# Performance work log

Measured on AMD Instinct MI355X. Metric: run time of the kernel, lower is better.

The kernel has to match this reference:

```python
import jax, jax.numpy as jnp
import numpy as np

K = 64  # init kwarg k
B, D = 4096, 16384


def setup_inputs() -> dict:
    key = jax.random.key(0)
    x = jax.random.normal(key, (B, D), dtype=jnp.float32)
    return {"x": x}


def reference(x):
    # top-k along last dim, then scatter values into a zero tensor (same as
    # torch.topk + zeros_like + scatter_).
    vals, idx = jax.lax.top_k(x, K)            # [B, K], [B, K]
    rows = jnp.arange(x.shape[0])[:, None]     # [B, 1] broadcast against idx
    return jnp.zeros_like(x).at[rows, idx].set(vals)
```

## Files before the change

kernel.cpp:

```cpp
#include <hip/hip_runtime.h>


#define TK_D      16384
#define TK_K      64
#define TK_BLOCK  512
#define TK_NV     8
#define TK_BINS   2048
#define TK_CAP    1024

__device__ __forceinline__ unsigned ord_map(unsigned b) {
    return b ^ ((unsigned)((int)b >> 31) | 0x80000000u);
}
__device__ __forceinline__ unsigned ord_inv(unsigned u) {
    return u ^ ((unsigned)((int)(~u) >> 31) | 0x80000000u);
}

__launch_bounds__(TK_BLOCK, 4)
__global__ void topk_scatter_kernel(const float* __restrict__ x,
                                    float* __restrict__ out) {
    __shared__ int      sh_hist[TK_BINS];
    __shared__ int      sh_wsum[8];
    __shared__ unsigned sh_cu[TK_CAP];
    __shared__ int      sh_cidx[TK_CAP];
    __shared__ int      sh_bin;
    __shared__ int      sh_rem;
    __shared__ int      sh_cnt;
    __shared__ unsigned sh_T;
    __shared__ int      sh_need;

    const int row  = blockIdx.x;
    const int tid  = threadIdx.x;
    const int lane = tid & 63;
    const int wv   = tid >> 6;

    const uint4* __restrict__ xr = (const uint4*)(x + (size_t)row * TK_D);
    uint4 r[TK_NV];
    #pragma unroll
    for (int i = 0; i < TK_NV; i++) r[i] = xr[tid + i * TK_BLOCK];

    ((int4*)sh_hist)[tid] = int4{0, 0, 0, 0};
    if (tid == 0) sh_cnt = 0;

    #pragma unroll
    for (int i = 0; i < TK_NV; i++) {
        r[i].x = ord_map(r[i].x);
        r[i].y = ord_map(r[i].y);
        r[i].z = ord_map(r[i].z);
        r[i].w = ord_map(r[i].w);
    }
    __syncthreads();

    #pragma unroll
    for (int i = 0; i < TK_NV; i++) {
        #pragma unroll
        for (int c = 0; c < 4; c++) {
            unsigned u = ((const unsigned*)&r[i])[c];
            atomicAdd(&sh_hist[u >> 21], 1);
        }
    }
    __syncthreads();

    int h0 = sh_hist[4 * tid + 0], h1 = sh_hist[4 * tid + 1];
    int h2 = sh_hist[4 * tid + 2], h3 = sh_hist[4 * tid + 3];
    int local = h0 + h1 + h2 + h3;
    int suf = local;
    #pragma unroll
    for (int off = 1; off < 64; off <<= 1) {
        int o = __shfl_down(suf, off);
        if (lane + off < 64) suf += o;
    }
    if (lane == 0) sh_wsum[wv] = suf;
    __syncthreads();

    int above = 0;
    #pragma unroll
    for (int w2 = 0; w2 < 8; w2++)
        if (w2 > wv) above += sh_wsum[w2];

    int a3 = above + (suf - local);
    int S3 = a3 + h3, S2 = S3 + h2, S1 = S2 + h1, S0 = S1 + h0;
    if      (S3 >= TK_K && a3 < TK_K) { sh_bin = 4 * tid + 3; sh_rem = TK_K - a3; }
    else if (S2 >= TK_K && S3 < TK_K) { sh_bin = 4 * tid + 2; sh_rem = TK_K - S3; }
    else if (S1 >= TK_K && S2 < TK_K) { sh_bin = 4 * tid + 1; sh_rem = TK_K - S2; }
    else if (S0 >= TK_K && S1 < TK_K) { sh_bin = 4 * tid + 0; sh_rem = TK_K - S1; }
    __syncthreads();

    const unsigned binv = (unsigned)sh_bin;
    const int      rem  = sh_rem;

    #pragma unroll
    for (int i = 0; i < TK_NV; i++) {
        #pragma unroll
        for (int c = 0; c < 4; c++) {
            unsigned u = ((const unsigned*)&r[i])[c];
            if ((u >> 21) == binv) {
                int pos = atomicAdd(&sh_cnt, 1);
                if (pos < TK_CAP) {
                    sh_cu[pos]   = u;
                    sh_cidx[pos] = 4 * (tid + i * TK_BLOCK) + c;
                }
            }
        }
    }
    __syncthreads();

    const int C = min(sh_cnt, TK_CAP);
    for (int i = tid; i < C; i += TK_BLOCK) {
        unsigned ui = sh_cu[i];
        int abv = 0, eq = 0;
        for (int j = 0; j < C; j++) {
            unsigned uj = sh_cu[j];
            abv += (uj > ui);
            eq  += (uj == ui);
        }
        if (abv < rem && abv + eq >= rem) {
            sh_T    = ui;
            sh_need = rem - abv;
        }
    }
    __syncthreads();

    const unsigned T    = sh_T;
    const int      need = sh_need;

    float4* __restrict__ orow = (float4*)(out + (size_t)row * TK_D);
    #pragma unroll
    for (int i = 0; i < TK_NV; i++) {
        float4 o;
        #pragma unroll
        for (int c = 0; c < 4; c++) {
            unsigned u = ((const unsigned*)&r[i])[c];
            ((float*)&o)[c] = (u > T) ? __uint_as_float(ord_inv(u)) : 0.0f;
        }
        orow[tid + i * TK_BLOCK] = o;
    }
    __syncthreads();

    const float tval = __uint_as_float(ord_inv(T));
    for (int i = tid; i < C; i += TK_BLOCK) {
        if (sh_cu[i] == T) {
            int col  = sh_cidx[i];
            int rank = 0;
            for (int j = 0; j < C; j++)
                rank += (sh_cu[j] == T && sh_cidx[j] < col);
            if (rank < need)
                out[(size_t)row * TK_D + col] = tval;
        }
    }
}

extern "C" void kernel_launch(void* const* d_in, const int* in_sizes, int n_in,
                              void* d_out, int out_size, void* d_ws, size_t ws_size,
                              hipStream_t stream) {
    const float* x = (const float*)d_in[0];
    float* out = (float*)d_out;
    const int B = in_sizes[0] / TK_D;
    topk_scatter_kernel<<<B, TK_BLOCK, 0, stream>>>(x, out);
}
```

Measured before the change: 441.8 us.

## Use persistent blocks with double-buffered register prefetch of next row

Launches a fixed grid of 512 persistent blocks that each loop over rows, prefetching the next row into a second register buffer while the current row is processed. Barriers become raw s_barrier calls that wait only on LDS counters, so the outstanding global prefetch loads are not drained at each barrier. The tie-handling scatter is folded into the main output write. Holding two row buffers doubles register pressure and may cut occupancy. Rows are assumed divisible by the grid size, and there is no barrier between rows before shared memory is reused.

```diff
diff --git a/kernel.cpp b/kernel.cpp
--- a/kernel.cpp
+++ b/kernel.cpp
@@ -5,6 +5,7 @@
 #define TK_K      64
 #define TK_BLOCK  512
 #define TK_NV     8
+#define TK_GRID   512
 #define TK_BINS   2048
 #define TK_CAP    1024
 
@@ -15,53 +16,45 @@
     return u ^ ((unsigned)((int)(~u) >> 31) | 0x80000000u);
 }
 
-__launch_bounds__(TK_BLOCK, 4)
-__global__ void topk_scatter_kernel(const float* __restrict__ x,
-                                    float* __restrict__ out) {
-    __shared__ int      sh_hist[TK_BINS];
-    __shared__ int      sh_wsum[8];
-    __shared__ unsigned sh_cu[TK_CAP];
-    __shared__ int      sh_cidx[TK_CAP];
-    __shared__ int      sh_bin;
-    __shared__ int      sh_rem;
-    __shared__ int      sh_cnt;
-    __shared__ unsigned sh_T;
-    __shared__ int      sh_need;
+__device__ __forceinline__ void bar_lds() {
+    asm volatile("s_waitcnt lgkmcnt(0)" ::: "memory");
+    __builtin_amdgcn_s_barrier();
+    asm volatile("" ::: "memory");
+}
 
-    const int row  = blockIdx.x;
-    const int tid  = threadIdx.x;
-    const int lane = tid & 63;
-    const int wv   = tid >> 6;
+struct TkShared {
+    int      hist[TK_BINS];
+    int      wsum[8];
+    unsigned cu[TK_CAP];
+    int      cidx[TK_CAP];
+    int      bin, rem, cnt, need;
+    unsigned T;
+};
 
-    const uint4* __restrict__ xr = (const uint4*)(x + (size_t)row * TK_D);
-    uint4 r[TK_NV];
+__device__ __forceinline__ void process_row(uint4 (&b)[TK_NV], int row,
+                                            float* __restrict__ out,
+                                            TkShared& sh,
+                                            int tid, int lane, int wv) {
     #pragma unroll
-    for (int i = 0; i < TK_NV; i++) r[i] = xr[tid + i * TK_BLOCK];
-
-    ((int4*)sh_hist)[tid] = int4{0, 0, 0, 0};
-    if (tid == 0) sh_cnt = 0;
+    for (int i = 0; i < TK_NV; i++) {
+        b[i].x = ord_map(b[i].x); b[i].y = ord_map(b[i].y);
+        b[i].z = ord_map(b[i].z); b[i].w = ord_map(b[i].w);
+    }
+    ((int4*)sh.hist)[tid] = int4{0, 0, 0, 0};
+    if (tid == 0) sh.cnt = 0;
+    bar_lds();
 
     #pragma unroll
     for (int i = 0; i < TK_NV; i++) {
-        r[i].x = ord_map(r[i].x);
-        r[i].y = ord_map(r[i].y);
-        r[i].z = ord_map(r[i].z);
-        r[i].w = ord_map(r[i].w);
+        atomicAdd(&sh.hist[b[i].x >> 21], 1);
+        atomicAdd(&sh.hist[b[i].y >> 21], 1);
+        atomicAdd(&sh.hist[b[i].z >> 21], 1);
+        atomicAdd(&sh.hist[b[i].w >> 21], 1);
     }
-    __syncthreads();
+    bar_lds();
 
-    #pragma unroll
-    for (int i = 0; i < TK_NV; i++) {
-        #pragma unroll
-        for (int c = 0; c < 4; c++) {
-            unsigned u = ((const unsigned*)&r[i])[c];
-            atomicAdd(&sh_hist[u >> 21], 1);
-        }
-    }
-    __syncthreads();
-
-    int h0 = sh_hist[4 * tid + 0], h1 = sh_hist[4 * tid + 1];
-    int h2 = sh_hist[4 * tid + 2], h3 = sh_hist[4 * tid + 3];
+    int h0 = sh.hist[4 * tid + 0], h1 = sh.hist[4 * tid + 1];
+    int h2 = sh.hist[4 * tid + 2], h3 = sh.hist[4 * tid + 3];
     int local = h0 + h1 + h2 + h3;
     int suf = local;
     #pragma unroll
@@ -69,59 +62,59 @@
         int o = __shfl_down(suf, off);
         if (lane + off < 64) suf += o;
     }
-    if (lane == 0) sh_wsum[wv] = suf;
-    __syncthreads();
+    if (lane == 0) sh.wsum[wv] = suf;
+    bar_lds();
 
     int above = 0;
     #pragma unroll
     for (int w2 = 0; w2 < 8; w2++)
-        if (w2 > wv) above += sh_wsum[w2];
-
+        if (w2 > wv) above += sh.wsum[w2];
     int a3 = above + (suf - local);
     int S3 = a3 + h3, S2 = S3 + h2, S1 = S2 + h1, S0 = S1 + h0;
-    if      (S3 >= TK_K && a3 < TK_K) { sh_bin = 4 * tid + 3; sh_rem = TK_K - a3; }
-    else if (S2 >= TK_K && S3 < TK_K) { sh_bin = 4 * tid + 2; sh_rem = TK_K - S3; }
-    else if (S1 >= TK_K && S2 < TK_K) { sh_bin = 4 * tid + 1; sh_rem = TK_K - S2; }
-    else if (S0 >= TK_K && S1 < TK_K) { sh_bin = 4 * tid + 0; sh_rem = TK_K - S1; }
-    __syncthreads();
+    if      (S3 >= TK_K && a3 < TK_K) { sh.bin = 4 * tid + 3; sh.rem = TK_K - a3; }
+    else if (S2 >= TK_K && S3 < TK_K) { sh.bin = 4 * tid + 2; sh.rem = TK_K - S3; }
+    else if (S1 >= TK_K && S2 < TK_K) { sh.bin = 4 * tid + 1; sh.rem = TK_K - S2; }
+    else if (S0 >= TK_K && S1 < TK_K) { sh.bin = 4 * tid + 0; sh.rem = TK_K - S1; }
+    bar_lds();
 
-    const unsigned binv = (unsigned)sh_bin;
-    const int      rem  = sh_rem;
+    const unsigned binv = (unsigned)sh.bin;
+    const int      rem  = sh.rem;
 
     #pragma unroll
     for (int i = 0; i < TK_NV; i++) {
         #pragma unroll
         for (int c = 0; c < 4; c++) {
-            unsigned u = ((const unsigned*)&r[i])[c];
+            unsigned u = ((const unsigned*)&b[i])[c];
             if ((u >> 21) == binv) {
-                int pos = atomicAdd(&sh_cnt, 1);
+                int pos = atomicAdd(&sh.cnt, 1);
                 if (pos < TK_CAP) {
-                    sh_cu[pos]   = u;
-                    sh_cidx[pos] = 4 * (tid + i * TK_BLOCK) + c;
+                    sh.cu[pos]   = u;
+                    sh.cidx[pos] = 4 * (tid + i * TK_BLOCK) + c;
                 }
             }
         }
     }
-    __syncthreads();
+    bar_lds();
 
-    const int C = min(sh_cnt, TK_CAP);
+    const int C = min(sh.cnt, TK_CAP);
     for (int i = tid; i < C; i += TK_BLOCK) {
-        unsigned ui = sh_cu[i];
+        unsigned ui = sh.cu[i];
         int abv = 0, eq = 0;
         for (int j = 0; j < C; j++) {
-            unsigned uj = sh_cu[j];
+            unsigned uj = sh.cu[j];
             abv += (uj > ui);
             eq  += (uj == ui);
         }
         if (abv < rem && abv + eq >= rem) {
-            sh_T    = ui;
-            sh_need = rem - abv;
+            sh.T    = ui;
+            sh.need = rem - abv;
         }
     }
-    __syncthreads();
+    bar_lds();
 
-    const unsigned T    = sh_T;
-    const int      need = sh_need;
+    const unsigned T    = sh.T;
+    const int      need = sh.need;
+    const float    tval = __uint_as_float(ord_inv(T));
 
     float4* __restrict__ orow = (float4*)(out + (size_t)row * TK_D);
     #pragma unroll
@@ -129,22 +122,55 @@
         float4 o;
         #pragma unroll
         for (int c = 0; c < 4; c++) {
-            unsigned u = ((const unsigned*)&r[i])[c];
-            ((float*)&o)[c] = (u > T) ? __uint_as_float(ord_inv(u)) : 0.0f;
+            unsigned u = ((const unsigned*)&b[i])[c];
+            float v = (u > T) ? __uint_as_float(ord_inv(u)) : 0.0f;
+            if (u == T) {
+                int col  = 4 * (tid + i * TK_BLOCK) + c;
+                int rank = 0;
+                for (int j = 0; j < C; j++)
+                    rank += (sh.cu[j] == T && sh.cidx[j] < col);
+                v = (rank < need) ? tval : 0.0f;
+            }
+            ((float*)&o)[c] = v;
         }
         orow[tid + i * TK_BLOCK] = o;
     }
-    __syncthreads();
+}
 
-    const float tval = __uint_as_float(ord_inv(T));
-    for (int i = tid; i < C; i += TK_BLOCK) {
-        if (sh_cu[i] == T) {
-            int col  = sh_cidx[i];
-            int rank = 0;
-            for (int j = 0; j < C; j++)
-                rank += (sh_cu[j] == T && sh_cidx[j] < col);
-            if (rank < need)
-                out[(size_t)row * TK_D + col] = tval;
+__launch_bounds__(TK_BLOCK, 4)
+__global__ void topk_scatter_kernel(const float* __restrict__ x,
+                                    float* __restrict__ out, int nrows) {
+    __shared__ TkShared sh;
+    const int tid  = threadIdx.x;
+    const int lane = tid & 63;
+    const int wv   = tid >> 6;
+    const int niter = nrows / TK_GRID;
+
+    uint4 bufA[TK_NV], bufB[TK_NV];
+    int rowA = blockIdx.x;
+    {
+        const uint4* __restrict__ p = (const uint4*)(x + (size_t)rowA * TK_D);
+        #pragma unroll
+        for (int i = 0; i < TK_NV; i++) bufA[i] = p[tid + i * TK_BLOCK];
+    }
+    #pragma unroll 1
+    for (int it = 0; it < niter; it += 2) {
+        const int rowB = rowA + TK_GRID;
+        if (it + 1 < niter) {
+            const uint4* __restrict__ p = (const uint4*)(x + (size_t)rowB * TK_D);
+            #pragma unroll
+            for (int i = 0; i < TK_NV; i++) bufB[i] = p[tid + i * TK_BLOCK];
+        }
+        process_row(bufA, rowA, out, sh, tid, lane, wv);
+        if (it + 1 < niter) {
+            const int rowA2 = rowB + TK_GRID;
+            if (it + 2 < niter) {
+                const uint4* __restrict__ p = (const uint4*)(x + (size_t)rowA2 * TK_D);
+                #pragma unroll
+                for (int i = 0; i < TK_NV; i++) bufA[i] = p[tid + i * TK_BLOCK];
+            }
+            process_row(bufB, rowB, out, sh, tid, lane, wv);
+            rowA = rowA2;
         }
     }
 }
@@ -155,5 +181,5 @@
     const float* x = (const float*)d_in[0];
     float* out = (float*)d_out;
     const int B = in_sizes[0] / TK_D;
-    topk_scatter_kernel<<<B, TK_BLOCK, 0, stream>>>(x, out);
+    topk_scatter_kernel<<<TK_GRID, TK_BLOCK, 0, stream>>>(x, out, B);
 }
```

Measured after the change: 514.5 us. +16.5%, slower.

## Use persistent blocks with next-row prefetch and coverage-masked output writes

Applied to the files above, without the earlier changes.

The kernel becomes persistent: a fixed grid of 512 blocks loops over rows, and each block loads the next row into registers while it runs the candidate-ranking phase of the current row. Elements above the threshold bin are recorded in a small LDS list. Threshold-bin candidates get their final values written directly, and the dense store writes zeros only for lanes not already covered. The aim is to hide global load latency and remove the extra final pass, at the cost of scattered writes, a rows-divisible-by-grid assumption, and a 64-entry winner cap.

```diff
diff --git a/kernel.cpp b/kernel.cpp
--- a/kernel.cpp
+++ b/kernel.cpp
@@ -5,8 +5,10 @@
 #define TK_K      64
 #define TK_BLOCK  512
 #define TK_NV     8
+#define TK_GRID   512
 #define TK_BINS   2048
 #define TK_CAP    1024
+#define TK_WCAP   64
 
 __device__ __forceinline__ unsigned ord_map(unsigned b) {
     return b ^ ((unsigned)((int)b >> 31) | 0x80000000u);
@@ -15,136 +17,169 @@
     return u ^ ((unsigned)((int)(~u) >> 31) | 0x80000000u);
 }
 
+__device__ __forceinline__ void bar_lds() {
+    asm volatile("s_waitcnt lgkmcnt(0)" ::: "memory");
+    __builtin_amdgcn_s_barrier();
+    asm volatile("" ::: "memory");
+}
+
 __launch_bounds__(TK_BLOCK, 4)
 __global__ void topk_scatter_kernel(const float* __restrict__ x,
-                                    float* __restrict__ out) {
+                                    float* __restrict__ out, int nrows) {
     __shared__ int      sh_hist[TK_BINS];
     __shared__ int      sh_wsum[8];
     __shared__ unsigned sh_cu[TK_CAP];
     __shared__ int      sh_cidx[TK_CAP];
-    __shared__ int      sh_bin;
-    __shared__ int      sh_rem;
-    __shared__ int      sh_cnt;
+    __shared__ unsigned sh_wval[TK_WCAP];
+    __shared__ int      sh_wcol[TK_WCAP];
+    __shared__ int      sh_bin, sh_rem, sh_cnt, sh_wcnt, sh_need;
     __shared__ unsigned sh_T;
-    __shared__ int      sh_need;
 
-    const int row  = blockIdx.x;
-    const int tid  = threadIdx.x;
-    const int lane = tid & 63;
-    const int wv   = tid >> 6;
+    const int tid   = threadIdx.x;
+    const int lane  = tid & 63;
+    const int wv    = tid >> 6;
+    const int niter = nrows / TK_GRID;
 
-    const uint4* __restrict__ xr = (const uint4*)(x + (size_t)row * TK_D);
-    uint4 r[TK_NV];
-    #pragma unroll
-    for (int i = 0; i < TK_NV; i++) r[i] = xr[tid + i * TK_BLOCK];
+    uint4 b[TK_NV];
+    {
+        const uint4* __restrict__ p = (const uint4*)(x + (size_t)blockIdx.x * TK_D);
+        #pragma unroll
+        for (int i = 0; i < TK_NV; i++) b[i] = p[tid + i * TK_BLOCK];
+    }
 
-    ((int4*)sh_hist)[tid] = int4{0, 0, 0, 0};
-    if (tid == 0) sh_cnt = 0;
+    #pragma unroll 1
+    for (int it = 0; it < niter; it++) {
+        const int row = blockIdx.x + it * TK_GRID;
 
-    #pragma unroll
-    for (int i = 0; i < TK_NV; i++) {
-        r[i].x = ord_map(r[i].x);
-        r[i].y = ord_map(r[i].y);
-        r[i].z = ord_map(r[i].z);
-        r[i].w = ord_map(r[i].w);
-    }
-    __syncthreads();
+        #pragma unroll
+        for (int i = 0; i < TK_NV; i++) {
+            b[i].x = ord_map(b[i].x); b[i].y = ord_map(b[i].y);
+            b[i].z = ord_map(b[i].z); b[i].w = ord_map(b[i].w);
+        }
+        ((int4*)sh_hist)[tid] = int4{0, 0, 0, 0};
+        if (tid == 0) { sh_cnt = 0; sh_wcnt = 0; }
+        bar_lds();
 
-    #pragma unroll
-    for (int i = 0; i < TK_NV; i++) {
         #pragma unroll
-        for (int c = 0; c < 4; c++) {
-            unsigned u = ((const unsigned*)&r[i])[c];
-            atomicAdd(&sh_hist[u >> 21], 1);
+        for (int i = 0; i < TK_NV; i++) {
+            atomicAdd(&sh_hist[b[i].x >> 21], 1);
+            atomicAdd(&sh_hist[b[i].y >> 21], 1);
+            atomicAdd(&sh_hist[b[i].z >> 21], 1);
+            atomicAdd(&sh_hist[b[i].w >> 21], 1);
         }
-    }
-    __syncthreads();
+        bar_lds();
 
-    int h0 = sh_hist[4 * tid + 0], h1 = sh_hist[4 * tid + 1];
-    int h2 = sh_hist[4 * tid + 2], h3 = sh_hist[4 * tid + 3];
-    int local = h0 + h1 + h2 + h3;
-    int suf = local;
-    #pragma unroll
-    for (int off = 1; off < 64; off <<= 1) {
-        int o = __shfl_down(suf, off);
-        if (lane + off < 64) suf += o;
-    }
-    if (lane == 0) sh_wsum[wv] = suf;
-    __syncthreads();
+        int h0 = sh_hist[4 * tid + 0], h1 = sh_hist[4 * tid + 1];
+        int h2 = sh_hist[4 * tid + 2], h3 = sh_hist[4 * tid + 3];
+        int local = h0 + h1 + h2 + h3;
+        int suf = local;
+        #pragma unroll
+        for (int off = 1; off < 64; off <<= 1) {
+            int o = __shfl_down(suf, off);
+            if (lane + off < 64) suf += o;
+        }
+        if (lane == 0) sh_wsum[wv] = suf;
+        bar_lds();
 
-    int above = 0;
-    #pragma unroll
-    for (int w2 = 0; w2 < 8; w2++)
-        if (w2 > wv) above += sh_wsum[w2];
+        int above = 0;
+        #pragma unroll
+        for (int w2 = 0; w2 < 8; w2++)
+            if (w2 > wv) above += sh_wsum[w2];
+        int a3 = above + (suf - local);
+        int S3 = a3 + h3, S2 = S3 + h2, S1 = S2 + h1, S0 = S1 + h0;
+        if      (S3 >= TK_K && a3 < TK_K) { sh_bin = 4 * tid + 3; sh_rem = TK_K - a3; }
+        else if (S2 >= TK_K && S3 < TK_K) { sh_bin = 4 * tid + 2; sh_rem = TK_K - S3; }
+        else if (S1 >= TK_K && S2 < TK_K) { sh_bin = 4 * tid + 1; sh_rem = TK_K - S2; }
+        else if (S0 >= TK_K && S1 < TK_K) { sh_bin = 4 * tid + 0; sh_rem = TK_K - S1; }
+        bar_lds();
 
-    int a3 = above + (suf - local);
-    int S3 = a3 + h3, S2 = S3 + h2, S1 = S2 + h1, S0 = S1 + h0;
-    if      (S3 >= TK_K && a3 < TK_K) { sh_bin = 4 * tid + 3; sh_rem = TK_K - a3; }
-    else if (S2 >= TK_K && S3 < TK_K) { sh_bin = 4 * tid + 2; sh_rem = TK_K - S3; }
-    else if (S1 >= TK_K && S2 < TK_K) { sh_bin = 4 * tid + 1; sh_rem = TK_K - S2; }
-    else if (S0 >= TK_K && S1 < TK_K) { sh_bin = 4 * tid + 0; sh_rem = TK_K - S1; }
-    __syncthreads();
+        const unsigned binv = (unsigned)sh_bin;
+        const int      rem  = sh_rem;
 
-    const unsigned binv = (unsigned)sh_bin;
-    const int      rem  = sh_rem;
-
-    #pragma unroll
-    for (int i = 0; i < TK_NV; i++) {
+        unsigned mcov = 0u;
         #pragma unroll
-        for (int c = 0; c < 4; c++) {
-            unsigned u = ((const unsigned*)&r[i])[c];
-            if ((u >> 21) == binv) {
-                int pos = atomicAdd(&sh_cnt, 1);
-                if (pos < TK_CAP) {
-                    sh_cu[pos]   = u;
-                    sh_cidx[pos] = 4 * (tid + i * TK_BLOCK) + c;
+        for (int i = 0; i < TK_NV; i++) {
+            #pragma unroll
+            for (int c = 0; c < 4; c++) {
+                unsigned u  = ((const unsigned*)&b[i])[c];
+                unsigned bn = u >> 21;
+                if (bn > binv) {
+                    int pos = atomicAdd(&sh_wcnt, 1);
+                    if (pos < TK_WCAP) {
+                        sh_wval[pos] = u;
+                        sh_wcol[pos] = 4 * (tid + i * TK_BLOCK) + c;
+                    }
+                    mcov |= 1u << (4 * i + c);
+                } else if (bn == binv) {
+                    int pos = atomicAdd(&sh_cnt, 1);
+                    if (pos < TK_CAP) {
+                        sh_cu[pos]   = u;
+                        sh_cidx[pos] = 4 * (tid + i * TK_BLOCK) + c;
+                        mcov |= 1u << (4 * i + c);
+                    }
                 }
             }
         }
-    }
-    __syncthreads();
+        bar_lds();
 
-    const int C = min(sh_cnt, TK_CAP);
-    for (int i = tid; i < C; i += TK_BLOCK) {
-        unsigned ui = sh_cu[i];
-        int abv = 0, eq = 0;
-        for (int j = 0; j < C; j++) {
-            unsigned uj = sh_cu[j];
-            abv += (uj > ui);
-            eq  += (uj == ui);
+        const int C = min(sh_cnt, TK_CAP);
+        const int W = min(sh_wcnt, TK_WCAP);
+
+        if (it + 1 < niter) {
+            const uint4* __restrict__ p =
+                (const uint4*)(x + (size_t)(row + TK_GRID) * TK_D);
+            #pragma unroll
+            for (int i = 0; i < TK_NV; i++) b[i] = p[tid + i * TK_BLOCK];
         }
-        if (abv < rem && abv + eq >= rem) {
-            sh_T    = ui;
-            sh_need = rem - abv;
+
+        for (int i = tid; i < C; i += TK_BLOCK) {
+            unsigned ui = sh_cu[i];
+            int abv = 0, eq = 0;
+            for (int j = 0; j < C; j++) {
+                unsigned uj = sh_cu[j];
+                abv += (uj > ui);
+                eq  += (uj == ui);
+            }
+            if (abv < rem && abv + eq >= rem) {
+                sh_T    = ui;
+                sh_need = rem - abv;
+            }
         }
-    }
-    __syncthreads();
+        bar_lds();
 
-    const unsigned T    = sh_T;
-    const int      need = sh_need;
+        const unsigned T    = sh_T;
+        const int      need = sh_need;
+        const float    tval = __uint_as_float(ord_inv(T));
 
-    float4* __restrict__ orow = (float4*)(out + (size_t)row * TK_D);
-    #pragma unroll
-    for (int i = 0; i < TK_NV; i++) {
-        float4 o;
+        float* const orow = out + (size_t)row * TK_D;
         #pragma unroll
-        for (int c = 0; c < 4; c++) {
-            unsigned u = ((const unsigned*)&r[i])[c];
-            ((float*)&o)[c] = (u > T) ? __uint_as_float(ord_inv(u)) : 0.0f;
+        for (int i = 0; i < TK_NV; i++) {
+            const int q = tid + i * TK_BLOCK;
+            const unsigned qm = (mcov >> (4 * i)) & 0xFu;
+            if (qm == 0u) {
+                ((float4*)orow)[q] = float4{0.0f, 0.0f, 0.0f, 0.0f};
+            } else {
+                #pragma unroll
+                for (int c = 0; c < 4; c++)
+                    if (!((qm >> c) & 1u)) orow[4 * q + c] = 0.0f;
+            }
         }
-        orow[tid + i * TK_BLOCK] = o;
-    }
-    __syncthreads();
 
-    const float tval = __uint_as_float(ord_inv(T));
-    for (int i = tid; i < C; i += TK_BLOCK) {
-        if (sh_cu[i] == T) {
-            int col  = sh_cidx[i];
-            int rank = 0;
-            for (int j = 0; j < C; j++)
-                rank += (sh_cu[j] == T && sh_cidx[j] < col);
-            if (rank < need)
-                out[(size_t)row * TK_D + col] = tval;
+        for (int i = tid; i < W; i += TK_BLOCK)
+            orow[sh_wcol[i]] = __uint_as_float(ord_inv(sh_wval[i]));
+        for (int i = tid; i < C; i += TK_BLOCK) {
+            unsigned u   = sh_cu[i];
+            int      col = sh_cidx[i];
+            float v = 0.0f;
+            if (u > T) {
+                v = __uint_as_float(ord_inv(u));
+            } else if (u == T) {
+                int rank = 0;
+                for (int j = 0; j < C; j++)
+                    rank += (sh_cu[j] == T && sh_cidx[j] < col);
+                if (rank < need) v = tval;
+            }
+            orow[col] = v;
         }
     }
 }
@@ -155,5 +190,5 @@
     const float* x = (const float*)d_in[0];
     float* out = (float*)d_out;
     const int B = in_sizes[0] / TK_D;
-    topk_scatter_kernel<<<B, TK_BLOCK, 0, stream>>>(x, out);
+    topk_scatter_kernel<<<TK_GRID, TK_BLOCK, 0, stream>>>(x, out, B);
 }
```

Measured after the change: 470.2 us. +6.4%, slower.

## Split top-k into select kernel writing pairs and separate dense write kernel

Applied to the files above, without the earlier changes.

The single fused kernel becomes two. The first selects the top-k elements and writes (column, value) pairs into the head of each output row. The second reads those pairs, builds the dense row in shared memory and writes it out. The likely aim is to shorten the register-heavy select kernel and separate the zero-fill writes from the selection work. The cost is an extra launch, an extra round-trip through global memory, a 64 KB shared buffer in the write kernel that limits occupancy, and correctness that depends on the kernels running in order on the stream.

```diff
diff --git a/kernel.cpp b/kernel.cpp
--- a/kernel.cpp
+++ b/kernel.cpp
@@ -7,6 +7,7 @@
 #define TK_NV     8
 #define TK_BINS   2048
 #define TK_CAP    1024
+#define TK_WCAP   64
 
 __device__ __forceinline__ unsigned ord_map(unsigned b) {
     return b ^ ((unsigned)((int)b >> 31) | 0x80000000u);
@@ -16,47 +17,43 @@
 }
 
 __launch_bounds__(TK_BLOCK, 4)
-__global__ void topk_scatter_kernel(const float* __restrict__ x,
-                                    float* __restrict__ out) {
+__global__ void topk_select_kernel(const float* __restrict__ x,
+                                   float* __restrict__ out) {
     __shared__ int      sh_hist[TK_BINS];
     __shared__ int      sh_wsum[8];
     __shared__ unsigned sh_cu[TK_CAP];
     __shared__ int      sh_cidx[TK_CAP];
-    __shared__ int      sh_bin;
-    __shared__ int      sh_rem;
-    __shared__ int      sh_cnt;
+    __shared__ unsigned sh_wval[TK_WCAP];
+    __shared__ int      sh_wcol[TK_WCAP];
+    __shared__ int      sh_bin, sh_rem, sh_cnt, sh_wcnt, sh_need, sh_emit;
     __shared__ unsigned sh_T;
-    __shared__ int      sh_need;
 
     const int row  = blockIdx.x;
     const int tid  = threadIdx.x;
     const int lane = tid & 63;
     const int wv   = tid >> 6;
 
-    const uint4* __restrict__ xr = (const uint4*)(x + (size_t)row * TK_D);
-    uint4 r[TK_NV];
-    #pragma unroll
-    for (int i = 0; i < TK_NV; i++) r[i] = xr[tid + i * TK_BLOCK];
-
+    uint4 b[TK_NV];
+    {
+        const uint4* __restrict__ p = (const uint4*)(x + (size_t)row * TK_D);
+        #pragma unroll
+        for (int i = 0; i < TK_NV; i++) b[i] = p[tid + i * TK_BLOCK];
+    }
     ((int4*)sh_hist)[tid] = int4{0, 0, 0, 0};
-    if (tid == 0) sh_cnt = 0;
-
+    if (tid == 0) { sh_cnt = 0; sh_wcnt = 0; sh_emit = 0; }
     #pragma unroll
     for (int i = 0; i < TK_NV; i++) {
-        r[i].x = ord_map(r[i].x);
-        r[i].y = ord_map(r[i].y);
-        r[i].z = ord_map(r[i].z);
-        r[i].w = ord_map(r[i].w);
+        b[i].x = ord_map(b[i].x); b[i].y = ord_map(b[i].y);
+        b[i].z = ord_map(b[i].z); b[i].w = ord_map(b[i].w);
     }
     __syncthreads();
 
     #pragma unroll
     for (int i = 0; i < TK_NV; i++) {
-        #pragma unroll
-        for (int c = 0; c < 4; c++) {
-            unsigned u = ((const unsigned*)&r[i])[c];
-            atomicAdd(&sh_hist[u >> 21], 1);
-        }
+        atomicAdd(&sh_hist[b[i].x >> 21], 1);
+        atomicAdd(&sh_hist[b[i].y >> 21], 1);
+        atomicAdd(&sh_hist[b[i].z >> 21], 1);
+        atomicAdd(&sh_hist[b[i].w >> 21], 1);
     }
     __syncthreads();
 
@@ -76,7 +73,6 @@
     #pragma unroll
     for (int w2 = 0; w2 < 8; w2++)
         if (w2 > wv) above += sh_wsum[w2];
-
     int a3 = above + (suf - local);
     int S3 = a3 + h3, S2 = S3 + h2, S1 = S2 + h1, S0 = S1 + h0;
     if      (S3 >= TK_K && a3 < TK_K) { sh_bin = 4 * tid + 3; sh_rem = TK_K - a3; }
@@ -92,8 +88,15 @@
     for (int i = 0; i < TK_NV; i++) {
         #pragma unroll
         for (int c = 0; c < 4; c++) {
-            unsigned u = ((const unsigned*)&r[i])[c];
-            if ((u >> 21) == binv) {
+            unsigned u  = ((const unsigned*)&b[i])[c];
+            unsigned bn = u >> 21;
+            if (bn > binv) {
+                int pos = atomicAdd(&sh_wcnt, 1);
+                if (pos < TK_WCAP) {
+                    sh_wval[pos] = u;
+                    sh_wcol[pos] = 4 * (tid + i * TK_BLOCK) + c;
+                }
+            } else if (bn == binv) {
                 int pos = atomicAdd(&sh_cnt, 1);
                 if (pos < TK_CAP) {
                     sh_cu[pos]   = u;
@@ -105,6 +108,8 @@
     __syncthreads();
 
     const int C = min(sh_cnt, TK_CAP);
+    const int W = min(sh_wcnt, TK_WCAP);
+
     for (int i = tid; i < C; i += TK_BLOCK) {
         unsigned ui = sh_cu[i];
         int abv = 0, eq = 0;
@@ -123,29 +128,56 @@
     const unsigned T    = sh_T;
     const int      need = sh_need;
 
-    float4* __restrict__ orow = (float4*)(out + (size_t)row * TK_D);
+    float2* const prow = (float2*)(out + (size_t)row * TK_D);
+    for (int i = tid; i < W; i += TK_BLOCK) {
+        int s = atomicAdd(&sh_emit, 1);
+        prow[s] = float2{__uint_as_float((unsigned)sh_wcol[i]),
+                         __uint_as_float(ord_inv(sh_wval[i]))};
+    }
+    for (int i = tid; i < C; i += TK_BLOCK) {
+        unsigned u = sh_cu[i];
+        bool take = (u > T);
+        if (u == T) {
+            int col = sh_cidx[i], rank = 0;
+            for (int j = 0; j < C; j++)
+                rank += (sh_cu[j] == T && sh_cidx[j] < col);
+            take = (rank < need);
+        }
+        if (take) {
+            int s = atomicAdd(&sh_emit, 1);
+            prow[s] = float2{__uint_as_float((unsigned)sh_cidx[i]),
+                             __uint_as_float(ord_inv(u))};
+        }
+    }
+}
+
+__launch_bounds__(TK_BLOCK, 4)
+__global__ void topk_write_kernel(float* __restrict__ out) {
+    __shared__ float sh_row[TK_D];
+    __shared__ int   sh_col[TK_K];
+    __shared__ float sh_val[TK_K];
+
+    const int row = blockIdx.x;
+    const int tid = threadIdx.x;
+    float* const orow = out + (size_t)row * TK_D;
+
+    if (tid < TK_K) {
+        float2 pr = ((const float2*)orow)[tid];
+        sh_col[tid] = (int)__float_as_uint(pr.x);
+        sh_val[tid] = pr.y;
+    }
+    #pragma unroll
+    for (int i = 0; i < TK_NV; i++)
+        ((float4*)sh_row)[tid + i * TK_BLOCK] = float4{0.f, 0.f, 0.f, 0.f};
+    __syncthreads();
+
+    if (tid < TK_K) sh_row[sh_col[tid]] = sh_val[tid];
+    __syncthreads();
+
     #pragma unroll
     for (int i = 0; i < TK_NV; i++) {
-        float4 o;
-        #pragma unroll
-        for (int c = 0; c < 4; c++) {
-            unsigned u = ((const unsigned*)&r[i])[c];
-            ((float*)&o)[c] = (u > T) ? __uint_as_float(ord_inv(u)) : 0.0f;
-        }
-        orow[tid + i * TK_BLOCK] = o;
-    }
-    __syncthreads();
-
-    const float tval = __uint_as_float(ord_inv(T));
-    for (int i = tid; i < C; i += TK_BLOCK) {
-        if (sh_cu[i] == T) {
-            int col  = sh_cidx[i];
-            int rank = 0;
-            for (int j = 0; j < C; j++)
-                rank += (sh_cu[j] == T && sh_cidx[j] < col);
-            if (rank < need)
-                out[(size_t)row * TK_D + col] = tval;
-        }
+        float4 v = ((const float4*)sh_row)[tid + i * TK_BLOCK];
+        ((float4*)orow)[tid + i * TK_BLOCK] = v;
     }
 }
 
@@ -155,5 +187,6 @@
     const float* x = (const float*)d_in[0];
     float* out = (float*)d_out;
     const int B = in_sizes[0] / TK_D;
-    topk_scatter_kernel<<<B, TK_BLOCK, 0, stream>>>(x, out);
+    topk_select_kernel<<<B, TK_BLOCK, 0, stream>>>(x, out);
+    topk_write_kernel<<<B, TK_BLOCK, 0, stream>>>(out);
 }
```

After: 455.8 us. 1.03x slower.
